# Kernel tuning notes

Hardware: AMD Instinct MI355X
Metric: run time of the kernel (lower is better)

## Reference

```python
import jax, jax.numpy as jnp
import numpy as np
import math

C = 32            # multiplicity of 0e and 1o in edge_feats / target irreps
SQRT3 = math.sqrt(3.0)

def _mlp(s, W1, W2, W3):
    # e3nn haiku MLP: bias-free linears with 1/sqrt(fan_in) forward scaling,
    # activation between hidden layers, no output activation.
    h = jax.nn.silu(s @ (W1 / math.sqrt(W1.shape[0])))
    h = jax.nn.silu(h @ (W2 / math.sqrt(W2.shape[0])))
    return h @ (W3 / math.sqrt(W3.shape[0]))

def reference(edge_feats, edge_attrs, receivers, n_nodes, W1, W2, W3):
    E = edge_feats.shape[0]
    # split irreps: edge_feats = 32x0e ++ 32x1o ; edge_attrs = 1x0e ++ 1x1o
    s = edge_feats[:, :C]                       # [E, 32]   scalars (0e)
    v = edge_feats[:, C:].reshape(E, C, 3)      # [E, 32, 3] vectors (1o)
    s0 = edge_attrs[:, :1]                      # [E, 1]
    v0 = edge_attrs[:, 1:4]                     # [E, 3]

    # full tensor product filtered to 0e + 1o (component normalization):
    #   0e x 0e -> 0e : s*s0
    #   1o x 1o -> 0e : dot(v, v0)/sqrt(3)
    #   0e x 1o -> 1o : s*v0
    #   1o x 0e -> 1o : v*s0
    msg_s = jnp.concatenate([s * s0,
                             jnp.einsum('ecd,ed->ec', v, v0) / SQRT3], axis=-1)  # [E, 64]
    msg_v = jnp.concatenate([s[:, :, None] * v0[:, None, :],
                             v * s0[:, :, None]], axis=1)                        # [E, 64, 3]

    # MLP gate from scalar (0e) part of edge_feats -> one scalar per output irrep
    mix = _mlp(s, W1, W2, W3)                   # [E, 128] = 64 (0e) + 64 (1o)
    msg_s = msg_s * mix[:, :2 * C]
    msg_v = msg_v * mix[:, 2 * C:, None]

    # scatter-sum aggregate over receivers
    agg_s = jax.ops.segment_sum(msg_s, receivers, num_segments=n_nodes)  # [N, 64]
    agg_v = jax.ops.segment_sum(msg_v, receivers, num_segments=n_nodes)  # [N, 64, 3]

    node_feats = jnp.concatenate([agg_s, agg_v.reshape(n_nodes, -1)], axis=-1)  # [N, 256]
    return node_feats / jnp.sqrt(jnp.asarray(20.0, node_feats.dtype))

def setup_inputs() -> dict:
    key = jax.random.key(0)
    k1, k2, k3, k4, k5, k6 = jax.random.split(key, 6)
    E, N = 500000, 25000
    return {
        'edge_feats': jax.random.normal(k1, (E, 128), jnp.float32),
        'edge_attrs': jax.random.normal(k2, (E, 4), jnp.float32),
        'receivers': jax.random.randint(k3, (E,), 0, N),
        'n_nodes': N,
        'W1': jax.random.normal(k4, (32, 64), jnp.float32),
        'W2': jax.random.normal(k5, (64, 64), jnp.float32),
        'W3': jax.random.normal(k6, (64, 128), jnp.float32),
    }
```

## Files before the change

kernel.cpp:

```cpp
#include <hip/hip_runtime.h>
#include <stdint.h>


#define NCH 256

constexpr float INV_SQRT32 = 0.17677669529663687f;
constexpr float INV_8      = 0.125f;
constexpr float INV_SQRT3  = 0.57735026918962576f;
constexpr float SCALE      = 0.22360679774997896f;

typedef _Float16 h2_t __attribute__((ext_vector_type(2)));

__device__ __forceinline__ float f4c(const float4 v, int c) {
    return c == 0 ? v.x : c == 1 ? v.y : c == 2 ? v.z : v.w;
}
__device__ __forceinline__ unsigned int bf16_rne(float f) {
    unsigned int u = __float_as_uint(f);
    return (u + 0x7fffu + ((u >> 16) & 1u)) >> 16;
}
__device__ __forceinline__ unsigned int pack2(float a, float b) {
    return bf16_rne(a) | (bf16_rne(b) << 16);
}
__device__ __forceinline__ float bl(unsigned int u) { return __uint_as_float(u << 16); }
__device__ __forceinline__ float bh(unsigned int u) { return __uint_as_float(u & 0xffff0000u); }

__device__ __forceinline__ unsigned int packh2(float a, float b) {
    h2_t v; v[0] = (_Float16)a; v[1] = (_Float16)b;
    return __builtin_bit_cast(unsigned int, v);
}
__device__ __forceinline__ float dot2u(unsigned int a, unsigned int b, float c) {
#if __has_builtin(__builtin_amdgcn_fdot2)
    return __builtin_amdgcn_fdot2(__builtin_bit_cast(h2_t, a),
                                  __builtin_bit_cast(h2_t, b), c, false);
#else
    h2_t x = __builtin_bit_cast(h2_t, a), y = __builtin_bit_cast(h2_t, b);
    return fmaf((float)x[0], (float)y[0], fmaf((float)x[1], (float)y[1], c));
#endif
}

__global__ void wconv_kernel(const float* __restrict__ W1, const float* __restrict__ W2,
                             const float* __restrict__ W3, unsigned int* __restrict__ wp) {
    int t = blockIdx.x * 256 + threadIdx.x;
    if (t < 1024) {
        int k = t >> 6, j = t & 63;
        wp[t] = packh2(W1[2 * k * 64 + j], W1[(2 * k + 1) * 64 + j]);
    } else if (t < 3072) {
        int i = t - 1024, k = i >> 6, j = i & 63;
        wp[t] = packh2(W2[2 * k * 64 + j], W2[(2 * k + 1) * 64 + j]);
    } else if (t < 5120) {
        int i = t - 3072, k = i >> 6, j = i & 63;
        wp[t] = packh2(W3[2 * k * 128 + j], W3[(2 * k + 1) * 128 + j]);
    } else if (t < 7168) {
        int i = t - 5120, k = i >> 6, j = i & 63;
        wp[t] = packh2(W3[2 * k * 128 + 64 + j], W3[(2 * k + 1) * 128 + 64 + j]);
    }
}

__global__ void hist_kernel(const int* __restrict__ recv, int* __restrict__ cnt, int E) {
    int e = blockIdx.x * 256 + threadIdx.x;
    if (e < E) atomicAdd(&cnt[recv[e]], 1);
}

__global__ __launch_bounds__(1024) void scan_kernel(const int* __restrict__ cnt,
                                                    int* __restrict__ off, int N) {
    __shared__ int sh[1024];
    __shared__ int sbase;
    if (threadIdx.x == 0) sbase = 0;
    __syncthreads();
    for (int base = 0; base < N; base += 1024) {
        int i = base + threadIdx.x;
        int v = (i < N) ? cnt[i] : 0;
        sh[threadIdx.x] = v;
        __syncthreads();
        #pragma unroll
        for (int d = 1; d < 1024; d <<= 1) {
            int t = (threadIdx.x >= d) ? sh[threadIdx.x - d] : 0;
            __syncthreads();
            sh[threadIdx.x] += t;
            __syncthreads();
        }
        int incl = sh[threadIdx.x];
        int bb = sbase;
        if (i < N) off[i] = bb + incl - v;
        __syncthreads();
        if (threadIdx.x == 1023) sbase = bb + incl;
        __syncthreads();
    }
    if (threadIdx.x == 0) off[N] = sbase;
}

__global__ __launch_bounds__(256, 2) void msg_kernel(
    const float* __restrict__ edge_feats,
    const float* __restrict__ edge_attrs,
    const int*   __restrict__ receivers,
    const unsigned int* __restrict__ wp,
    const int* __restrict__ off, int* __restrict__ cursor, int* __restrict__ perm,
    unsigned int* __restrict__ msg,
    int E)
{
    __shared__ unsigned int hp[32][256];

    const unsigned int* wp1  = wp;
    const unsigned int* wp2  = wp + 1024;
    const unsigned int* wp3a = wp + 3072;
    const unsigned int* wp3b = wp + 5120;

    const int tid = threadIdx.x;
    const int e = blockIdx.x * 256 + tid;
    const bool valid = (e < E);
    const int ec = valid ? e : (E - 1);
    const float4* row4 = (const float4*)(edge_feats + (size_t)ec * 128);

    const float4 ea = *(const float4*)(edge_attrs + (size_t)ec * 4);
    const float s0 = ea.x, v0x = ea.y, v0y = ea.z, v0z = ea.w;

    if (valid) {
        const int r = receivers[e];
        const int pos = off[r] + atomicAdd(&cursor[r], 1);
        perm[pos] = e;
    }

    float acc[64];

    #pragma unroll
    for (int j = 0; j < 64; ++j) acc[j] = 0.f;
    #pragma unroll
    for (int kk = 0; kk < 8; ++kk) {
        const float4 r4 = row4[kk];
        const unsigned int p0 = packh2(r4.x, r4.y);
        const unsigned int p1 = packh2(r4.z, r4.w);
        const unsigned int* w = wp1 + kk * 128;
        #pragma unroll
        for (int j = 0; j < 64; ++j) acc[j] = dot2u(p0, w[j], acc[j]);
        #pragma unroll
        for (int j = 0; j < 64; ++j) acc[j] = dot2u(p1, w[64 + j], acc[j]);
    }
    #pragma unroll
    for (int p = 0; p < 32; ++p) {
        float x0 = acc[2 * p] * INV_SQRT32;     x0 = x0 / (1.f + __expf(-x0));
        float x1 = acc[2 * p + 1] * INV_SQRT32; x1 = x1 / (1.f + __expf(-x1));
        hp[p][tid] = packh2(x0, x1);
    }

    #pragma unroll
    for (int j = 0; j < 64; ++j) acc[j] = 0.f;
    for (int k = 0; k < 32; ++k) {
        const unsigned int u = hp[k][tid];
        const unsigned int* w = wp2 + k * 64;
        #pragma unroll
        for (int j = 0; j < 64; ++j) acc[j] = dot2u(u, w[j], acc[j]);
    }
    #pragma unroll
    for (int p = 0; p < 32; ++p) {
        float x0 = acc[2 * p] * INV_8;     x0 = x0 / (1.f + __expf(-x0));
        float x1 = acc[2 * p + 1] * INV_8; x1 = x1 / (1.f + __expf(-x1));
        hp[p][tid] = packh2(x0, x1);
    }

    uint4* mp = (uint4*)(msg + (size_t)ec * 128);

    #pragma unroll
    for (int j = 0; j < 64; ++j) acc[j] = 0.f;
    for (int k = 0; k < 32; ++k) {
        const unsigned int u = hp[k][tid];
        const unsigned int* w = wp3a + k * 64;
        #pragma unroll
        for (int j = 0; j < 64; ++j) acc[j] = dot2u(u, w[j], acc[j]);
    }
    float4 rv[8];
    #pragma unroll
    for (int i = 0; i < 8; ++i) rv[i] = row4[i];

    {
        unsigned int arr[32];
        #pragma unroll
        for (int w = 0; w < 16; ++w) {
            const int c0 = 2 * w, c1 = c0 + 1;
            const float a = f4c(rv[c0 >> 2], c0 & 3) * s0 * acc[c0] * (INV_8 * SCALE);
            const float b = f4c(rv[c1 >> 2], c1 & 3) * s0 * acc[c1] * (INV_8 * SCALE);
            arr[w] = pack2(a, b);
        }
        #pragma unroll
        for (int g = 0; g < 8; ++g) {
            const float4 q0 = row4[8 + 3 * g], q1 = row4[8 + 3 * g + 1], q2 = row4[8 + 3 * g + 2];
            const float d0 = q0.x * v0x + q0.y * v0y + q0.z * v0z;
            const float d1 = q0.w * v0x + q1.x * v0y + q1.y * v0z;
            const float d2 = q1.z * v0x + q1.w * v0y + q2.x * v0z;
            const float d3 = q2.y * v0x + q2.z * v0y + q2.w * v0z;
            const float sc = INV_8 * SCALE * INV_SQRT3;
            arr[16 + 2 * g]     = pack2(d0 * acc[32 + 4 * g] * sc,     d1 * acc[32 + 4 * g + 1] * sc);
            arr[16 + 2 * g + 1] = pack2(d2 * acc[32 + 4 * g + 2] * sc, d3 * acc[32 + 4 * g + 3] * sc);
        }
        if (valid) {
            #pragma unroll
            for (int q = 0; q < 8; ++q)
                mp[q] = make_uint4(arr[4 * q], arr[4 * q + 1], arr[4 * q + 2], arr[4 * q + 3]);
        }
    }

    #pragma unroll
    for (int j = 0; j < 64; ++j) acc[j] = 0.f;
    for (int k = 0; k < 32; ++k) {
        const unsigned int u = hp[k][tid];
        const unsigned int* w = wp3b + k * 64;
        #pragma unroll
        for (int j = 0; j < 64; ++j) acc[j] = dot2u(u, w[j], acc[j]);
    }
    {
        unsigned int arr2[48];
        #pragma unroll
        for (int w = 0; w < 48; ++w) {
            const int f0 = 2 * w, f1 = f0 + 1;
            const int j0 = f0 / 3, dd0 = f0 % 3, j1 = f1 / 3, dd1 = f1 % 3;
            const float a = f4c(rv[j0 >> 2], j0 & 3) * acc[j0] * (INV_8 * SCALE) *
                            (dd0 == 0 ? v0x : dd0 == 1 ? v0y : v0z);
            const float b = f4c(rv[j1 >> 2], j1 & 3) * acc[j1] * (INV_8 * SCALE) *
                            (dd1 == 0 ? v0x : dd1 == 1 ? v0y : v0z);
            arr2[w] = pack2(a, b);
        }
        if (valid) {
            #pragma unroll
            for (int q = 0; q < 12; ++q)
                mp[8 + q] = make_uint4(arr2[4 * q], arr2[4 * q + 1], arr2[4 * q + 2], arr2[4 * q + 3]);
        }
        #pragma unroll
        for (int g = 0; g < 8; ++g) {
            const float4 q0 = row4[8 + 3 * g], q1 = row4[8 + 3 * g + 1], q2 = row4[8 + 3 * g + 2];
            const float f[12] = {q0.x, q0.y, q0.z, q0.w, q1.x, q1.y, q1.z, q1.w,
                                 q2.x, q2.y, q2.z, q2.w};
            #pragma unroll
            for (int p = 0; p < 6; ++p) {
                const int i0 = 2 * p, i1 = i0 + 1;
                const float a = f[i0] * s0 * acc[32 + (g * 12 + i0) / 3] * (INV_8 * SCALE);
                const float b = f[i1] * s0 * acc[32 + (g * 12 + i1) / 3] * (INV_8 * SCALE);
                arr2[6 * g + p] = pack2(a, b);
            }
        }
        if (valid) {
            #pragma unroll
            for (int q = 0; q < 12; ++q)
                mp[20 + q] = make_uint4(arr2[4 * q], arr2[4 * q + 1], arr2[4 * q + 2], arr2[4 * q + 3]);
        }
    }
}

__global__ __launch_bounds__(256) void gather_kernel(
    const unsigned short* __restrict__ msg, const int* __restrict__ off,
    const int* __restrict__ perm, float* __restrict__ out, int N)
{
    const int wid = threadIdx.x >> 6;
    const int lane = threadIdx.x & 63;
    const int n = blockIdx.x * 4 + wid;
    if (n >= N) return;
    const int beg = off[n], end = off[n + 1];
    float a0 = 0.f, a1 = 0.f, a2 = 0.f, a3 = 0.f;
    int i = beg;
    for (; i + 1 < end; i += 2) {
        const int e1 = perm[i], e2 = perm[i + 1];
        const uint2 va = *(const uint2*)(msg + (size_t)e1 * 256 + lane * 4);
        const uint2 vb = *(const uint2*)(msg + (size_t)e2 * 256 + lane * 4);
        a0 += bl(va.x) + bl(vb.x);
        a1 += bh(va.x) + bh(vb.x);
        a2 += bl(va.y) + bl(vb.y);
        a3 += bh(va.y) + bh(vb.y);
    }
    if (i < end) {
        const int e1 = perm[i];
        const uint2 va = *(const uint2*)(msg + (size_t)e1 * 256 + lane * 4);
        a0 += bl(va.x); a1 += bh(va.x); a2 += bl(va.y); a3 += bh(va.y);
    }
    *(float4*)(out + (size_t)n * NCH + lane * 4) = make_float4(a0, a1, a2, a3);
}

__global__ __launch_bounds__(256, 2) void mpconv_atomic_kernel(
    const float* __restrict__ edge_feats, const float* __restrict__ edge_attrs,
    const int* __restrict__ receivers,
    const float* __restrict__ W1, const float* __restrict__ W2, const float* __restrict__ W3,
    float* __restrict__ out, int E)
{
    __shared__ float hbuf[64][256];
    const int tid = threadIdx.x;
    const int e = blockIdx.x * 256 + tid;
    if (e >= E) return;
    const float* row = edge_feats + (size_t)e * 128;
    float acc[64];
    #pragma unroll
    for (int j = 0; j < 64; ++j) acc[j] = 0.f;
    for (int k = 0; k < 32; ++k) {
        const float sk = row[k];
        const float* w = W1 + k * 64;
        #pragma unroll
        for (int j = 0; j < 64; ++j) acc[j] = fmaf(sk, w[j], acc[j]);
    }
    #pragma unroll
    for (int j = 0; j < 64; ++j) {
        const float x = acc[j] * INV_SQRT32;
        hbuf[j][tid] = x / (1.f + __expf(-x));
    }
    #pragma unroll
    for (int j = 0; j < 64; ++j) acc[j] = 0.f;
    for (int k = 0; k < 64; ++k) {
        const float hk = hbuf[k][tid];
        const float* w = W2 + k * 64;
        #pragma unroll
        for (int j = 0; j < 64; ++j) acc[j] = fmaf(hk, w[j], acc[j]);
    }
    #pragma unroll
    for (int j = 0; j < 64; ++j) {
        const float x = acc[j] * INV_8;
        hbuf[j][tid] = x / (1.f + __expf(-x));
    }
    const float4 ea = *reinterpret_cast<const float4*>(edge_attrs + (size_t)e * 4);
    const float s0 = ea.x, v0x = ea.y, v0y = ea.z, v0z = ea.w;
    const int r = receivers[e];
    float* o = out + (size_t)r * NCH;
    #pragma unroll
    for (int j = 0; j < 64; ++j) acc[j] = 0.f;
    for (int k = 0; k < 64; ++k) {
        const float hk = hbuf[k][tid];
        const float* w = W3 + k * 128;
        #pragma unroll
        for (int j = 0; j < 64; ++j) acc[j] = fmaf(hk, w[j], acc[j]);
    }
    #pragma unroll
    for (int j = 0; j < 32; ++j)
        unsafeAtomicAdd(o + j, row[j] * s0 * acc[j] * (INV_8 * SCALE));
    #pragma unroll
    for (int j = 32; j < 64; ++j) {
        const float* vr = row + 32 + (j - 32) * 3;
        const float dot = vr[0] * v0x + vr[1] * v0y + vr[2] * v0z;
        unsafeAtomicAdd(o + j, dot * acc[j] * (INV_8 * SCALE * INV_SQRT3));
    }
    #pragma unroll
    for (int j = 0; j < 64; ++j) acc[j] = 0.f;
    for (int k = 0; k < 64; ++k) {
        const float hk = hbuf[k][tid];
        const float* w = W3 + k * 128 + 64;
        #pragma unroll
        for (int j = 0; j < 64; ++j) acc[j] = fmaf(hk, w[j], acc[j]);
    }
    #pragma unroll
    for (int j = 0; j < 32; ++j) {
        const float sj = row[j] * acc[j] * (INV_8 * SCALE);
        unsafeAtomicAdd(o + 64 + j * 3 + 0, sj * v0x);
        unsafeAtomicAdd(o + 64 + j * 3 + 1, sj * v0y);
        unsafeAtomicAdd(o + 64 + j * 3 + 2, sj * v0z);
    }
    #pragma unroll
    for (int j = 32; j < 64; ++j) {
        const float m = acc[j] * (INV_8 * SCALE) * s0;
        const float* vr = row + 32 + (j - 32) * 3;
        unsafeAtomicAdd(o + 64 + j * 3 + 0, vr[0] * m);
        unsafeAtomicAdd(o + 64 + j * 3 + 1, vr[1] * m);
        unsafeAtomicAdd(o + 64 + j * 3 + 2, vr[2] * m);
    }
}

extern "C" void kernel_launch(void* const* d_in, const int* in_sizes, int n_in,
                              void* d_out, int out_size, void* d_ws, size_t ws_size,
                              hipStream_t stream) {
    const float* edge_feats = (const float*)d_in[0];
    const float* edge_attrs = (const float*)d_in[1];
    const int*   receivers  = (const int*)d_in[2];
    const float* W1 = (const float*)d_in[4];
    const float* W2 = (const float*)d_in[5];
    const float* W3 = (const float*)d_in[6];

    const int E = in_sizes[0] / 128;
    const int N = out_size / NCH;

    const size_t msg_bytes = (size_t)E * NCH * sizeof(unsigned short);
    const size_t need = msg_bytes + (size_t)(3 * N + 1 + E + 7168) * sizeof(int);

    if (ws_size >= need) {
        unsigned int* msg = (unsigned int*)d_ws;
        int* cnt    = (int*)((char*)d_ws + msg_bytes);
        int* cursor = cnt + N;
        int* off    = cursor + N;
        int* perm   = off + N + 1;
        unsigned int* wp = (unsigned int*)(perm + E);

        wconv_kernel<<<28, 256, 0, stream>>>(W1, W2, W3, wp);
        hipMemsetAsync(cnt, 0, (size_t)2 * N * sizeof(int), stream);
        hist_kernel<<<(E + 255) / 256, 256, 0, stream>>>(receivers, cnt, E);
        scan_kernel<<<1, 1024, 0, stream>>>(cnt, off, N);
        msg_kernel<<<(E + 255) / 256, 256, 0, stream>>>(
            edge_feats, edge_attrs, receivers, wp,
            off, cursor, perm, msg, E);
        gather_kernel<<<(N + 3) / 4, 256, 0, stream>>>(
            (const unsigned short*)msg, off, perm, (float*)d_out, N);
    } else {
        hipMemsetAsync(d_out, 0, (size_t)out_size * sizeof(float), stream);
        mpconv_atomic_kernel<<<(E + 255) / 256, 256, 0, stream>>>(
            edge_feats, edge_attrs, receivers, W1, W2, W3, (float*)d_out, E);
    }
}
```

Before: 486.7 us.

## Stage MLP weights in LDS, use 512-thread blocks, nontemporal message traffic

The message kernel now copies the packed fp16 MLP weights into shared memory in phases (W1+W2 first, then each W3 half) instead of reading them from global memory. Blocks grow to 512 threads with a larger shared activation buffer and a launch-bounds hint of four blocks per CU. SiLU uses a hardware reciprocal in place of a division, and the bf16 message writes and gather reads use nontemporal hints to keep them out of the caches. The extra barriers and weight reloads add synchronisation cost, and the tighter register budget from the new launch bounds may cause spills in the 64-accumulator loops.

Result: slower. 940.1 us (+93.2%).

```diff
diff --git a/kernel.cpp b/kernel.cpp
--- a/kernel.cpp
+++ b/kernel.cpp
@@ -10,6 +10,8 @@
 constexpr float SCALE      = 0.22360679774997896f;
 
 typedef _Float16 h2_t __attribute__((ext_vector_type(2)));
+typedef unsigned int u32x4 __attribute__((ext_vector_type(4)));
+typedef unsigned int u32x2 __attribute__((ext_vector_type(2)));
 
 __device__ __forceinline__ float f4c(const float4 v, int c) {
     return c == 0 ? v.x : c == 1 ? v.y : c == 2 ? v.z : v.w;
@@ -36,6 +38,19 @@
     h2_t x = __builtin_bit_cast(h2_t, a), y = __builtin_bit_cast(h2_t, b);
     return fmaf((float)x[0], (float)y[0], fmaf((float)x[1], (float)y[1], c));
 #endif
+}
+__device__ __forceinline__ float siluf(float x) {
+    const float d = 1.f + __expf(-x);
+#if __has_builtin(__builtin_amdgcn_rcpf)
+    return x * __builtin_amdgcn_rcpf(d);
+#else
+    return x / d;
+#endif
+}
+__device__ __forceinline__ void nt_store4(unsigned int* p, unsigned int a,
+                                          unsigned int b, unsigned int c, unsigned int d) {
+    u32x4 v; v[0] = a; v[1] = b; v[2] = c; v[3] = d;
+    __builtin_nontemporal_store(v, (u32x4*)p);
 }
 
 __global__ void wconv_kernel(const float* __restrict__ W1, const float* __restrict__ W2,
@@ -89,7 +104,7 @@
     if (threadIdx.x == 0) off[N] = sbase;
 }
 
-__global__ __launch_bounds__(256, 2) void msg_kernel(
+__global__ __launch_bounds__(512, 4) void msg_kernel(
     const float* __restrict__ edge_feats,
     const float* __restrict__ edge_attrs,
     const int*   __restrict__ receivers,
@@ -98,15 +113,21 @@
     unsigned int* __restrict__ msg,
     int E)
 {
-    __shared__ unsigned int hp[32][256];
-
-    const unsigned int* wp1  = wp;
-    const unsigned int* wp2  = wp + 1024;
-    const unsigned int* wp3a = wp + 3072;
-    const unsigned int* wp3b = wp + 5120;
+    __shared__ u32x4 wsh4[768];
+    __shared__ unsigned int hp[32][512];
+    unsigned int* wsh = (unsigned int*)wsh4;
 
     const int tid = threadIdx.x;
-    const int e = blockIdx.x * 256 + tid;
+    const u32x4* wp4 = (const u32x4*)wp;
+
+    #pragma unroll
+    for (int i = 0; i < 2; ++i) {
+        const int idx = i * 512 + tid;
+        if (idx < 768) wsh4[idx] = wp4[idx];
+    }
+    __syncthreads();
+
+    const int e = blockIdx.x * 512 + tid;
     const bool valid = (e < E);
     const int ec = valid ? e : (E - 1);
     const float4* row4 = (const float4*)(edge_feats + (size_t)ec * 128);
@@ -129,7 +150,7 @@
         const float4 r4 = row4[kk];
         const unsigned int p0 = packh2(r4.x, r4.y);
         const unsigned int p1 = packh2(r4.z, r4.w);
-        const unsigned int* w = wp1 + kk * 128;
+        const unsigned int* w = wsh + kk * 128;
         #pragma unroll
         for (int j = 0; j < 64; ++j) acc[j] = dot2u(p0, w[j], acc[j]);
         #pragma unroll
@@ -137,33 +158,35 @@
     }
     #pragma unroll
     for (int p = 0; p < 32; ++p) {
-        float x0 = acc[2 * p] * INV_SQRT32;     x0 = x0 / (1.f + __expf(-x0));
-        float x1 = acc[2 * p + 1] * INV_SQRT32; x1 = x1 / (1.f + __expf(-x1));
-        hp[p][tid] = packh2(x0, x1);
+        hp[p][tid] = packh2(siluf(acc[2 * p] * INV_SQRT32),
+                            siluf(acc[2 * p + 1] * INV_SQRT32));
     }
 
     #pragma unroll
     for (int j = 0; j < 64; ++j) acc[j] = 0.f;
     for (int k = 0; k < 32; ++k) {
         const unsigned int u = hp[k][tid];
-        const unsigned int* w = wp2 + k * 64;
+        const unsigned int* w = wsh + 1024 + k * 64;
         #pragma unroll
         for (int j = 0; j < 64; ++j) acc[j] = dot2u(u, w[j], acc[j]);
     }
     #pragma unroll
     for (int p = 0; p < 32; ++p) {
-        float x0 = acc[2 * p] * INV_8;     x0 = x0 / (1.f + __expf(-x0));
-        float x1 = acc[2 * p + 1] * INV_8; x1 = x1 / (1.f + __expf(-x1));
-        hp[p][tid] = packh2(x0, x1);
-    }
-
-    uint4* mp = (uint4*)(msg + (size_t)ec * 128);
+        hp[p][tid] = packh2(siluf(acc[2 * p] * INV_8),
+                            siluf(acc[2 * p + 1] * INV_8));
+    }
+
+    __syncthreads();
+    wsh4[tid] = wp4[768 + tid];
+    __syncthreads();
+
+    unsigned int* mp = msg + (size_t)ec * 128;
 
     #pragma unroll
     for (int j = 0; j < 64; ++j) acc[j] = 0.f;
     for (int k = 0; k < 32; ++k) {
         const unsigned int u = hp[k][tid];
-        const unsigned int* w = wp3a + k * 64;
+        const unsigned int* w = wsh + k * 64;
         #pragma unroll
         for (int j = 0; j < 64; ++j) acc[j] = dot2u(u, w[j], acc[j]);
     }
@@ -194,15 +217,19 @@
         if (valid) {
             #pragma unroll
             for (int q = 0; q < 8; ++q)
-                mp[q] = make_uint4(arr[4 * q], arr[4 * q + 1], arr[4 * q + 2], arr[4 * q + 3]);
-        }
-    }
+                nt_store4(mp + q * 4, arr[4 * q], arr[4 * q + 1], arr[4 * q + 2], arr[4 * q + 3]);
+        }
+    }
+
+    __syncthreads();
+    wsh4[tid] = wp4[1280 + tid];
+    __syncthreads();
 
     #pragma unroll
     for (int j = 0; j < 64; ++j) acc[j] = 0.f;
     for (int k = 0; k < 32; ++k) {
         const unsigned int u = hp[k][tid];
-        const unsigned int* w = wp3b + k * 64;
+        const unsigned int* w = wsh + k * 64;
         #pragma unroll
         for (int j = 0; j < 64; ++j) acc[j] = dot2u(u, w[j], acc[j]);
     }
@@ -221,7 +248,7 @@
         if (valid) {
             #pragma unroll
             for (int q = 0; q < 12; ++q)
-                mp[8 + q] = make_uint4(arr2[4 * q], arr2[4 * q + 1], arr2[4 * q + 2], arr2[4 * q + 3]);
+                nt_store4(mp + 32 + q * 4, arr2[4 * q], arr2[4 * q + 1], arr2[4 * q + 2], arr2[4 * q + 3]);
         }
         #pragma unroll
         for (int g = 0; g < 8; ++g) {
@@ -239,7 +266,7 @@
         if (valid) {
             #pragma unroll
             for (int q = 0; q < 12; ++q)
-                mp[20 + q] = make_uint4(arr2[4 * q], arr2[4 * q + 1], arr2[4 * q + 2], arr2[4 * q + 3]);
+                nt_store4(mp + 80 + q * 4, arr2[4 * q], arr2[4 * q + 1], arr2[4 * q + 2], arr2[4 * q + 3]);
         }
     }
 }
@@ -257,17 +284,20 @@
     int i = beg;
     for (; i + 1 < end; i += 2) {
         const int e1 = perm[i], e2 = perm[i + 1];
-        const uint2 va = *(const uint2*)(msg + (size_t)e1 * 256 + lane * 4);
-        const uint2 vb = *(const uint2*)(msg + (size_t)e2 * 256 + lane * 4);
-        a0 += bl(va.x) + bl(vb.x);
-        a1 += bh(va.x) + bh(vb.x);
-        a2 += bl(va.y) + bl(vb.y);
-        a3 += bh(va.y) + bh(vb.y);
+        const u32x2 va = __builtin_nontemporal_load(
+            (const u32x2*)(msg + (size_t)e1 * 256 + lane * 4));
+        const u32x2 vb = __builtin_nontemporal_load(
+            (const u32x2*)(msg + (size_t)e2 * 256 + lane * 4));
+        a0 += bl(va[0]) + bl(vb[0]);
+        a1 += bh(va[0]) + bh(vb[0]);
+        a2 += bl(va[1]) + bl(vb[1]);
+        a3 += bh(va[1]) + bh(vb[1]);
     }
     if (i < end) {
         const int e1 = perm[i];
-        const uint2 va = *(const uint2*)(msg + (size_t)e1 * 256 + lane * 4);
-        a0 += bl(va.x); a1 += bh(va.x); a2 += bl(va.y); a3 += bh(va.y);
+        const u32x2 va = __builtin_nontemporal_load(
+            (const u32x2*)(msg + (size_t)e1 * 256 + lane * 4));
+        a0 += bl(va[0]); a1 += bh(va[0]); a2 += bl(va[1]); a3 += bh(va[1]);
     }
     *(float4*)(out + (size_t)n * NCH + lane * 4) = make_float4(a0, a1, a2, a3);
 }
@@ -369,22 +399,23 @@
     const int E = in_sizes[0] / 128;
     const int N = out_size / NCH;
 
+    const size_t wb_bytes  = 7168 * sizeof(unsigned int);
     const size_t msg_bytes = (size_t)E * NCH * sizeof(unsigned short);
-    const size_t need = msg_bytes + (size_t)(3 * N + 1 + E + 7168) * sizeof(int);
+    const size_t need = wb_bytes + msg_bytes + (size_t)(3 * N + 1 + E) * sizeof(int);
 
     if (ws_size >= need) {
-        unsigned int* msg = (unsigned int*)d_ws;
-        int* cnt    = (int*)((char*)d_ws + msg_bytes);
+        unsigned int* wp  = (unsigned int*)d_ws;
+        unsigned int* msg = (unsigned int*)((char*)d_ws + wb_bytes);
+        int* cnt    = (int*)((char*)msg + msg_bytes);
         int* cursor = cnt + N;
         int* off    = cursor + N;
         int* perm   = off + N + 1;
-        unsigned int* wp = (unsigned int*)(perm + E);
 
         wconv_kernel<<<28, 256, 0, stream>>>(W1, W2, W3, wp);
         hipMemsetAsync(cnt, 0, (size_t)2 * N * sizeof(int), stream);
         hist_kernel<<<(E + 255) / 256, 256, 0, stream>>>(receivers, cnt, E);
         scan_kernel<<<1, 1024, 0, stream>>>(cnt, off, N);
-        msg_kernel<<<(E + 255) / 256, 256, 0, stream>>>(
+        msg_kernel<<<(E + 511) / 512, 512, 0, stream>>>(
             edge_feats, edge_attrs, receivers, wp,
             off, cursor, perm, msg, E);
         gather_kernel<<<(N + 3) / 4, 256, 0, stream>>>(
```
